# Performance work log

Measured on AMD Instinct MI355X. Metric: run time of the kernel, lower is better.

## Reference

```python
import jax, jax.numpy as jnp
import numpy as np

B, C, H, W = 2, 256, 96, 192
GROUPS = 4
K = 9  # search_window_1d = (1, 9) -> 9 candidates, x-offsets -4..4, y-offset 0


def bilinear_sample(img, coords):
    """F.grid_sample(mode='bilinear', padding_mode='zeros', align_corners=True)
    with absolute pixel coordinates (torchvision optical-flow grid_sample wrapper:
    normalize by 2*x/(W-1)-1 then grid_sample align_corners=True == identity mapping).
    img: [B, C, H, W]; coords: [B, Hg, Wg, 2] as (x, y). Returns [B, C, Hg, Wg]."""
    Bi, Ci, Hi, Wi = img.shape
    x = coords[..., 0]
    y = coords[..., 1]
    x0 = jnp.floor(x)
    y0 = jnp.floor(y)
    wx1 = x - x0
    wy1 = y - y0
    wx0 = 1.0 - wx1
    wy0 = 1.0 - wy1
    flat = img.reshape(Bi, Ci, Hi * Wi)

    def gather(ix, iy):
        valid = (ix >= 0) & (ix <= Wi - 1) & (iy >= 0) & (iy <= Hi - 1)
        ixc = jnp.clip(ix, 0, Wi - 1).astype(jnp.int32)
        iyc = jnp.clip(iy, 0, Hi - 1).astype(jnp.int32)
        idx = (iyc * Wi + ixc).reshape(Bi, 1, -1)  # [B,1,Hg*Wg]
        g = jnp.take_along_axis(flat, idx, axis=2)  # [B,C,Hg*Wg]
        g = g.reshape(Bi, Ci, *ix.shape[1:])
        return g * valid[:, None].astype(img.dtype)

    out = (gather(x0, y0) * (wx0 * wy0)[:, None]
           + gather(x0 + 1, y0) * (wx1 * wy0)[:, None]
           + gather(x0, y0 + 1) * (wx0 * wy1)[:, None]
           + gather(x0 + 1, y0 + 1) * (wx1 * wy1)[:, None])
    return out


def setup_inputs() -> dict:
    key = jax.random.key(0)
    k1, k2, k3, k4 = jax.random.split(key, 4)
    return {
        "left_feature": jax.random.normal(k1, (B, C, H, W), dtype=jnp.float32),
        "right_feature": jax.random.normal(k2, (B, C, H, W), dtype=jnp.float32),
        "flow": jax.random.normal(k3, (B, 2, H, W), dtype=jnp.float32),
        "extra_offset": jax.random.normal(k4, (B, 2 * K, H, W), dtype=jnp.float32),
    }


def reference(left_feature, right_feature, flow, extra_offset):
    Bf, Cf, Hf, Wf = left_feature.shape
    gc = Cf // GROUPS
    dt = left_feature.dtype
    # 1d window offsets: meshgrid(arange(-4,5), arange(0,1), 'xy') -> (x, 0) pairs
    xs = jnp.arange(-4, 5, dtype=dt)
    win_offs = jnp.stack([xs, jnp.zeros_like(xs)], axis=-1)  # [K,2] (x,y)
    # extra_offset: [B, K, 2, H, W] -> [B, K, H, W, 2]
    extra = extra_offset.reshape(Bf, K, 2, Hf, Wf).transpose(0, 1, 3, 4, 2)
    offsets = win_offs[None, :, None, None, :] + extra  # [B,K,H,W,2]
    # base coords grid (x, y) + flow
    yy, xx = jnp.meshgrid(jnp.arange(Hf), jnp.arange(Wf), indexing="ij")
    base = jnp.stack([xx, yy], axis=-1).astype(dt)  # [H,W,2]
    coords = base[None] + flow.transpose(0, 2, 3, 1)  # [B,H,W,2]
    coords = coords[:, None] + offsets  # [B,K,H,W,2]
    coords = coords.reshape(Bf, K * Hf, Wf, 2)
    # All groups share identical window/dilation -> sample full right feature once.
    sampled = bilinear_sample(right_feature, coords)  # [B,C,K*H,W]
    sampled = sampled.reshape(Bf, GROUPS, gc, K, Hf, Wf)
    left = left_feature.reshape(Bf, GROUPS, gc, 1, Hf, Wf)
    corr = jnp.mean(left * sampled, axis=2)  # [B,G,K,H,W]
    return corr.reshape(Bf, GROUPS * K, Hf, Wf)
```

## Files before the change

kernel.cpp:

```cpp
#include <hip/hip_runtime.h>


namespace {
constexpr int kB = 2;
constexpr int kC = 256;
constexpr int kH = 96;
constexpr int kW = 192;
constexpr int kG = 4;
constexpr int kGC = kC / kG;
constexpr int kK = 9;
constexpr int kHW = kH * kW;
constexpr size_t kPlane = (size_t)kC * kHW;
constexpr int kTransBlocks = (kHW / 64) * (kC / 64) * kB * 2;
constexpr int kPreBlocks   = (kB * kHW) / 256;
constexpr int kCorrBlocks  = kB * kHW / 8;
}

typedef _Float16 half8_t __attribute__((ext_vector_type(8)));
typedef _Float16 half4_t __attribute__((ext_vector_type(4)));
typedef _Float16 half2_t __attribute__((ext_vector_type(2)));

struct TapMeta {
  int4   off;
  float4 wgt;
};

__device__ __forceinline__ float dot8(half8_t a, half8_t b, float acc) {
#if __has_builtin(__builtin_amdgcn_fdot2)
  #pragma unroll
  for (int i = 0; i < 4; ++i) {
    half2_t a2 = {a[2 * i], a[2 * i + 1]};
    half2_t b2 = {b[2 * i], b[2 * i + 1]};
    acc = __builtin_amdgcn_fdot2(a2, b2, acc, false);
  }
#else
  #pragma unroll
  for (int i = 0; i < 8; ++i) acc += (float)a[i] * (float)b[i];
#endif
  return acc;
}

__global__ __launch_bounds__(256) void prepass_kernel(
    const float* __restrict__ left, const float* __restrict__ right,
    const float* __restrict__ flow, const float* __restrict__ extra,
    _Float16* __restrict__ left_t, _Float16* __restrict__ right_t,
    TapMeta* __restrict__ meta)
{
  __shared__ float tile[64][65];
  int id = blockIdx.x;
  if (id >= kPreBlocks) {
    int tb = id - kPreBlocks;
    int pt = tb % (kHW / 64);
    int ct = (tb / (kHW / 64)) % 4;
    int z  = tb / ((kHW / 64) * 4);
    int b  = z >> 1;
    const float* in = (z & 1) ? right : left;
    _Float16*   dst = (z & 1) ? right_t : left_t;
    int p0 = pt * 64, c0 = ct * 64;
    const float* inb = in + (size_t)b * kPlane;
    _Float16*   outb = dst + (size_t)b * kPlane;
    int t = threadIdx.x;
    int cl = t >> 2;
    int q  = t & 3;
    #pragma unroll
    for (int i = 0; i < 4; ++i) {
      int j = q + 4 * i;
      float4 v = *(const float4*)(inb + (size_t)(c0 + cl) * kHW + p0 + 4 * j);
      tile[cl][4 * j + 0] = v.x;
      tile[cl][4 * j + 1] = v.y;
      tile[cl][4 * j + 2] = v.z;
      tile[cl][4 * j + 3] = v.w;
    }
    __syncthreads();
    int pl = t >> 2;
    #pragma unroll
    for (int i = 0; i < 4; ++i) {
      int c4 = (t & 3) + 4 * i;
      half4_t hv;
      hv[0] = (_Float16)tile[4 * c4 + 0][pl];
      hv[1] = (_Float16)tile[4 * c4 + 1][pl];
      hv[2] = (_Float16)tile[4 * c4 + 2][pl];
      hv[3] = (_Float16)tile[4 * c4 + 3][pl];
      *(half4_t*)(outb + (size_t)(p0 + pl) * kC + c0 + 4 * c4) = hv;
    }
  } else {
    int t = id * 256 + threadIdx.x;
    int b = t / kHW, pix = t % kHW;
    int w = pix % kW, h = pix / kW;

    const float* flowb = flow + (size_t)b * 2 * kHW + pix;
    float bx = (float)w + flowb[0];
    float by = (float)h + flowb[kHW];
    const float* extb = extra + (size_t)b * 2 * kK * kHW + pix;

    TapMeta* mp = meta + (size_t)t * kK;
    #pragma unroll
    for (int k = 0; k < kK; ++k) {
      float xx = bx + (float)(k - 4) + extb[(size_t)(2 * k) * kHW];
      float yy = by + extb[(size_t)(2 * k + 1) * kHW];
      float xf = floorf(xx), yf = floorf(yy);
      float fx = xx - xf, fy = yy - yf;
      int ix0 = (int)xf, iy0 = (int)yf;
      int ix1 = ix0 + 1, iy1 = iy0 + 1;
      bool vx0 = (ix0 >= 0) && (ix0 < kW);
      bool vx1 = (ix1 >= 0) && (ix1 < kW);
      bool vy0 = (iy0 >= 0) && (iy0 < kH);
      bool vy1 = (iy1 >= 0) && (iy1 < kH);
      int xc0 = min(max(ix0, 0), kW - 1);
      int xc1 = min(max(ix1, 0), kW - 1);
      int yc0 = min(max(iy0, 0), kH - 1);
      int yc1 = min(max(iy1, 0), kH - 1);
      float wx0 = 1.f - fx, wy0 = 1.f - fy;
      TapMeta m;
      m.off.x = (yc0 * kW + xc0) * kC;
      m.off.y = (yc0 * kW + xc1) * kC;
      m.off.z = (yc1 * kW + xc0) * kC;
      m.off.w = (yc1 * kW + xc1) * kC;
      m.wgt.x = wx0 * wy0 * ((vx0 && vy0) ? 1.f : 0.f);
      m.wgt.y = fx  * wy0 * ((vx1 && vy0) ? 1.f : 0.f);
      m.wgt.z = wx0 * fy  * ((vx0 && vy1) ? 1.f : 0.f);
      m.wgt.w = fx  * fy  * ((vx1 && vy1) ? 1.f : 0.f);
      mp[k] = m;
    }
  }
}

__global__ __launch_bounds__(256) void corr_fp16_kernel(
    const _Float16* __restrict__ left_t, const _Float16* __restrict__ right_t,
    const TapMeta* __restrict__ meta, float* __restrict__ out)
{
  __shared__ TapMeta smeta[8 * kK];

  int sb = (blockIdx.x & 7) * (kCorrBlocks / 8) + (blockIdx.x >> 3);
  int blockPix = sb * 8;

  {
    const int4* src = (const int4*)(meta + (size_t)blockPix * kK);
    int4* dst = (int4*)smeta;
    int t = threadIdx.x;
    if (t < 144) dst[t] = src[t];
  }

  int wv   = threadIdx.x >> 6;
  int lane = threadIdx.x & 63;
  int base = blockPix + wv * 2;
  int b    = base / kHW;
  int pl0  = base % kHW;
  int p    = lane >> 5;
  int cl   = lane & 31;
  int pix  = pl0 + p;

  half8_t l8 = *(const half8_t*)(left_t + ((size_t)b * kHW + pix) * kC + cl * 8);

  const _Float16* Rb = right_t + (size_t)b * kPlane + cl * 8;

  __syncthreads();
  const TapMeta* mp = smeta + (wv * 2 + p) * kK;

  float rr[kK];

  #pragma unroll
  for (int kb = 0; kb < kK; kb += 3) {
    int4   off[3];
    float4 wv4[3];
    #pragma unroll
    for (int j = 0; j < 3; ++j) {
      off[j] = mp[kb + j].off;
      wv4[j] = mp[kb + j].wgt;
    }
    half8_t t[3][4];
    #pragma unroll
    for (int j = 0; j < 3; ++j) {
      t[j][0] = *(const half8_t*)(Rb + off[j].x);
      t[j][1] = *(const half8_t*)(Rb + off[j].y);
      t[j][2] = *(const half8_t*)(Rb + off[j].z);
      t[j][3] = *(const half8_t*)(Rb + off[j].w);
    }
    #pragma unroll
    for (int j = 0; j < 3; ++j) {
      float d00 = dot8(t[j][0], l8, 0.f);
      float d01 = dot8(t[j][1], l8, 0.f);
      float d10 = dot8(t[j][2], l8, 0.f);
      float d11 = dot8(t[j][3], l8, 0.f);
      float r = wv4[j].x * d00 + wv4[j].y * d01 + wv4[j].z * d10 + wv4[j].w * d11;
      r += __shfl_xor(r, 1);
      r += __shfl_xor(r, 2);
      r += __shfl_xor(r, 4);
      rr[kb + j] = r;
    }
  }

  int g = cl >> 3;
  if ((cl & 7) == 0) {
    float* outp = out + ((size_t)b * kG + g) * kK * kHW + pix;
    #pragma unroll
    for (int k = 0; k < kK; ++k)
      outp[(size_t)k * kHW] = rr[k] * (1.f / kGC);
  }
}

__global__ __launch_bounds__(256) void crestereo_corr_fallback(
    const float* __restrict__ left, const float* __restrict__ right,
    const float* __restrict__ flow, const float* __restrict__ extra,
    float* __restrict__ out)
{
  int t = blockIdx.x * blockDim.x + threadIdx.x;
  int w = t % kW;
  int h = (t / kW) % kH;
  int k = (t / kHW) % kK;
  int g = (t / (kHW * kK)) % kG;
  int b = t / (kHW * kK * kG);

  int pix = h * kW + w;
  const float* flowb = flow + b * 2 * kHW + pix;
  float x = (float)(w + (k - 4)) + flowb[0];
  float y = (float)h + flowb[kHW];
  const float* extb = extra + (size_t)(b * 2 * kK + 2 * k) * kHW + pix;
  x += extb[0];
  y += extb[kHW];

  float xf = floorf(x), yf = floorf(y);
  float fx = x - xf, fy = y - yf;
  int ix0 = (int)xf, iy0 = (int)yf;
  int ix1 = ix0 + 1, iy1 = iy0 + 1;
  bool vx0 = (ix0 >= 0) && (ix0 < kW);
  bool vx1 = (ix1 >= 0) && (ix1 < kW);
  bool vy0 = (iy0 >= 0) && (iy0 < kH);
  bool vy1 = (iy1 >= 0) && (iy1 < kH);
  int xc0 = min(max(ix0, 0), kW - 1);
  int xc1 = min(max(ix1, 0), kW - 1);
  int yc0 = min(max(iy0, 0), kH - 1);
  int yc1 = min(max(iy1, 0), kH - 1);
  float wx0 = 1.f - fx, wy0 = 1.f - fy;
  float w00 = wx0 * wy0 * ((vx0 && vy0) ? 1.f : 0.f);
  float w01 = fx  * wy0 * ((vx1 && vy0) ? 1.f : 0.f);
  float w10 = wx0 * fy  * ((vx0 && vy1) ? 1.f : 0.f);
  float w11 = fx  * fy  * ((vx1 && vy1) ? 1.f : 0.f);
  int idx = yc0 * kW + xc0;
  int dx  = xc1 - xc0;
  int dyw = (yc1 - yc0) * kW;

  const float* Rb = right + (size_t)(b * kC + g * kGC) * kHW + idx;
  const float* Lb = left  + (size_t)(b * kC + g * kGC) * kHW + pix;

  float acc = 0.f;
  #pragma unroll 4
  for (int c = 0; c < kGC; ++c) {
    const float* Rc = Rb + (size_t)c * kHW;
    float l   = Lb[(size_t)c * kHW];
    acc += l * (w00 * Rc[0] + w01 * Rc[dx] + w10 * Rc[dyw] + w11 * Rc[dx + dyw]);
  }
  out[(size_t)((b * kG + g) * kK + k) * kHW + pix] = acc * (1.f / kGC);
}

extern "C" void kernel_launch(void* const* d_in, const int* in_sizes, int n_in,
                              void* d_out, int out_size, void* d_ws, size_t ws_size,
                              hipStream_t stream) {
  const float* left  = (const float*)d_in[0];
  const float* right = (const float*)d_in[1];
  const float* flow  = (const float*)d_in[2];
  const float* extra = (const float*)d_in[3];
  float* out = (float*)d_out;

  size_t t_bytes = 2 * (size_t)kB * kPlane * sizeof(_Float16);
  size_t m_bytes = (size_t)kB * kHW * kK * sizeof(TapMeta);
  if (ws_size >= t_bytes + m_bytes) {
    _Float16* left_t  = (_Float16*)d_ws;
    _Float16* right_t = left_t + (size_t)kB * kPlane;
    TapMeta*  meta    = (TapMeta*)((char*)d_ws + t_bytes);

    prepass_kernel<<<kPreBlocks + kTransBlocks, 256, 0, stream>>>(
        left, right, flow, extra, left_t, right_t, meta);
    corr_fp16_kernel<<<kCorrBlocks, 256, 0, stream>>>(left_t, right_t, meta, out);
  } else {
    int total = kB * kG * kK * kH * kW;
    crestereo_corr_fallback<<<(total + 255) / 256, 256, 0, stream>>>(
        left, right, flow, extra, out);
  }
}
```

Baseline: 143.1 us.

## Compute tap metadata inside correlation kernel and widen transpose stores

Tap offsets and bilinear weights are now computed per block in the correlation kernel's shared memory, using 72 threads that each handle one (pixel, tap) pair. This replaces the global metadata buffer the prepass used to write and the correlation kernel used to re-read. The prepass becomes a pure transpose-and-convert kernel that writes 8-wide half vectors instead of 4-wide ones. This removes about 5 MB of metadata traffic and a block type from the prepass. In exchange, the correlation kernel does scattered flow/extra reads and computation before its barrier.

```diff
diff --git a/kernel.cpp b/kernel.cpp
--- a/kernel.cpp
+++ b/kernel.cpp
@@ -12,7 +12,6 @@
 constexpr int kHW = kH * kW;
 constexpr size_t kPlane = (size_t)kC * kHW;
 constexpr int kTransBlocks = (kHW / 64) * (kC / 64) * kB * 2;
-constexpr int kPreBlocks   = (kB * kHW) / 256;
 constexpr int kCorrBlocks  = kB * kHW / 8;
 }
 
@@ -42,115 +41,103 @@
 
 __global__ __launch_bounds__(256) void prepass_kernel(
     const float* __restrict__ left, const float* __restrict__ right,
-    const float* __restrict__ flow, const float* __restrict__ extra,
-    _Float16* __restrict__ left_t, _Float16* __restrict__ right_t,
-    TapMeta* __restrict__ meta)
+    _Float16* __restrict__ left_t, _Float16* __restrict__ right_t)
 {
   __shared__ float tile[64][65];
-  int id = blockIdx.x;
-  if (id >= kPreBlocks) {
-    int tb = id - kPreBlocks;
-    int pt = tb % (kHW / 64);
-    int ct = (tb / (kHW / 64)) % 4;
-    int z  = tb / ((kHW / 64) * 4);
-    int b  = z >> 1;
-    const float* in = (z & 1) ? right : left;
-    _Float16*   dst = (z & 1) ? right_t : left_t;
-    int p0 = pt * 64, c0 = ct * 64;
-    const float* inb = in + (size_t)b * kPlane;
-    _Float16*   outb = dst + (size_t)b * kPlane;
-    int t = threadIdx.x;
-    int cl = t >> 2;
-    int q  = t & 3;
-    #pragma unroll
-    for (int i = 0; i < 4; ++i) {
-      int j = q + 4 * i;
-      float4 v = *(const float4*)(inb + (size_t)(c0 + cl) * kHW + p0 + 4 * j);
-      tile[cl][4 * j + 0] = v.x;
-      tile[cl][4 * j + 1] = v.y;
-      tile[cl][4 * j + 2] = v.z;
-      tile[cl][4 * j + 3] = v.w;
-    }
-    __syncthreads();
-    int pl = t >> 2;
-    #pragma unroll
-    for (int i = 0; i < 4; ++i) {
-      int c4 = (t & 3) + 4 * i;
-      half4_t hv;
-      hv[0] = (_Float16)tile[4 * c4 + 0][pl];
-      hv[1] = (_Float16)tile[4 * c4 + 1][pl];
-      hv[2] = (_Float16)tile[4 * c4 + 2][pl];
-      hv[3] = (_Float16)tile[4 * c4 + 3][pl];
-      *(half4_t*)(outb + (size_t)(p0 + pl) * kC + c0 + 4 * c4) = hv;
-    }
-  } else {
-    int t = id * 256 + threadIdx.x;
-    int b = t / kHW, pix = t % kHW;
-    int w = pix % kW, h = pix / kW;
-
-    const float* flowb = flow + (size_t)b * 2 * kHW + pix;
+  int tb = blockIdx.x;
+  int pt = tb % (kHW / 64);
+  int ct = (tb / (kHW / 64)) % 4;
+  int z  = tb / ((kHW / 64) * 4);
+  int b  = z >> 1;
+  const float* in = (z & 1) ? right : left;
+  _Float16*   dst = (z & 1) ? right_t : left_t;
+  int p0 = pt * 64, c0 = ct * 64;
+  const float* inb = in + (size_t)b * kPlane;
+  _Float16*   outb = dst + (size_t)b * kPlane;
+  int t = threadIdx.x;
+  int cl = t >> 2;
+  int q  = t & 3;
+  #pragma unroll
+  for (int i = 0; i < 4; ++i) {
+    int j = q + 4 * i;
+    float4 v = *(const float4*)(inb + (size_t)(c0 + cl) * kHW + p0 + 4 * j);
+    tile[cl][4 * j + 0] = v.x;
+    tile[cl][4 * j + 1] = v.y;
+    tile[cl][4 * j + 2] = v.z;
+    tile[cl][4 * j + 3] = v.w;
+  }
+  __syncthreads();
+  int pl8 = t >> 3;
+  int c8  = t & 7;
+  #pragma unroll
+  for (int i = 0; i < 2; ++i) {
+    int px = pl8 + 32 * i;
+    half8_t hv;
+    #pragma unroll
+    for (int j = 0; j < 8; ++j)
+      hv[j] = (_Float16)tile[8 * c8 + j][px];
+    *(half8_t*)(outb + (size_t)(p0 + px) * kC + c0 + 8 * c8) = hv;
+  }
+}
+
+__global__ __launch_bounds__(256) void corr_fp16_kernel(
+    const _Float16* __restrict__ left_t, const _Float16* __restrict__ right_t,
+    const float* __restrict__ flow, const float* __restrict__ extra,
+    float* __restrict__ out)
+{
+  __shared__ TapMeta smeta[8 * kK];
+
+  int sb = (blockIdx.x & 7) * (kCorrBlocks / 8) + (blockIdx.x >> 3);
+  int blockPix = sb * 8;
+  int b    = blockPix / kHW;
+  int pix0 = blockPix % kHW;
+
+  int wv   = threadIdx.x >> 6;
+  int lane = threadIdx.x & 63;
+  int p    = lane >> 5;
+  int cl   = lane & 31;
+  int pix  = pix0 + wv * 2 + p;
+
+  half8_t l8 = *(const half8_t*)(left_t + ((size_t)b * kHW + pix) * kC + cl * 8);
+
+  int t = threadIdx.x;
+  if (t < 8 * kK) {
+    int px = t / kK;
+    int k  = t - px * kK;
+    int gpix = pix0 + px;
+    int w = gpix % kW, h = gpix / kW;
+
+    const float* flowb = flow + (size_t)b * 2 * kHW + gpix;
     float bx = (float)w + flowb[0];
     float by = (float)h + flowb[kHW];
-    const float* extb = extra + (size_t)b * 2 * kK * kHW + pix;
-
-    TapMeta* mp = meta + (size_t)t * kK;
-    #pragma unroll
-    for (int k = 0; k < kK; ++k) {
-      float xx = bx + (float)(k - 4) + extb[(size_t)(2 * k) * kHW];
-      float yy = by + extb[(size_t)(2 * k + 1) * kHW];
-      float xf = floorf(xx), yf = floorf(yy);
-      float fx = xx - xf, fy = yy - yf;
-      int ix0 = (int)xf, iy0 = (int)yf;
-      int ix1 = ix0 + 1, iy1 = iy0 + 1;
-      bool vx0 = (ix0 >= 0) && (ix0 < kW);
-      bool vx1 = (ix1 >= 0) && (ix1 < kW);
-      bool vy0 = (iy0 >= 0) && (iy0 < kH);
-      bool vy1 = (iy1 >= 0) && (iy1 < kH);
-      int xc0 = min(max(ix0, 0), kW - 1);
-      int xc1 = min(max(ix1, 0), kW - 1);
-      int yc0 = min(max(iy0, 0), kH - 1);
-      int yc1 = min(max(iy1, 0), kH - 1);
-      float wx0 = 1.f - fx, wy0 = 1.f - fy;
-      TapMeta m;
-      m.off.x = (yc0 * kW + xc0) * kC;
-      m.off.y = (yc0 * kW + xc1) * kC;
-      m.off.z = (yc1 * kW + xc0) * kC;
-      m.off.w = (yc1 * kW + xc1) * kC;
-      m.wgt.x = wx0 * wy0 * ((vx0 && vy0) ? 1.f : 0.f);
-      m.wgt.y = fx  * wy0 * ((vx1 && vy0) ? 1.f : 0.f);
-      m.wgt.z = wx0 * fy  * ((vx0 && vy1) ? 1.f : 0.f);
-      m.wgt.w = fx  * fy  * ((vx1 && vy1) ? 1.f : 0.f);
-      mp[k] = m;
-    }
-  }
-}
-
-__global__ __launch_bounds__(256) void corr_fp16_kernel(
-    const _Float16* __restrict__ left_t, const _Float16* __restrict__ right_t,
-    const TapMeta* __restrict__ meta, float* __restrict__ out)
-{
-  __shared__ TapMeta smeta[8 * kK];
-
-  int sb = (blockIdx.x & 7) * (kCorrBlocks / 8) + (blockIdx.x >> 3);
-  int blockPix = sb * 8;
-
-  {
-    const int4* src = (const int4*)(meta + (size_t)blockPix * kK);
-    int4* dst = (int4*)smeta;
-    int t = threadIdx.x;
-    if (t < 144) dst[t] = src[t];
-  }
-
-  int wv   = threadIdx.x >> 6;
-  int lane = threadIdx.x & 63;
-  int base = blockPix + wv * 2;
-  int b    = base / kHW;
-  int pl0  = base % kHW;
-  int p    = lane >> 5;
-  int cl   = lane & 31;
-  int pix  = pl0 + p;
-
-  half8_t l8 = *(const half8_t*)(left_t + ((size_t)b * kHW + pix) * kC + cl * 8);
+    const float* extb = extra + (size_t)b * 2 * kK * kHW + gpix;
+
+    float xx = bx + (float)(k - 4) + extb[(size_t)(2 * k) * kHW];
+    float yy = by + extb[(size_t)(2 * k + 1) * kHW];
+    float xf = floorf(xx), yf = floorf(yy);
+    float fx = xx - xf, fy = yy - yf;
+    int ix0 = (int)xf, iy0 = (int)yf;
+    int ix1 = ix0 + 1, iy1 = iy0 + 1;
+    bool vx0 = (ix0 >= 0) && (ix0 < kW);
+    bool vx1 = (ix1 >= 0) && (ix1 < kW);
+    bool vy0 = (iy0 >= 0) && (iy0 < kH);
+    bool vy1 = (iy1 >= 0) && (iy1 < kH);
+    int xc0 = min(max(ix0, 0), kW - 1);
+    int xc1 = min(max(ix1, 0), kW - 1);
+    int yc0 = min(max(iy0, 0), kH - 1);
+    int yc1 = min(max(iy1, 0), kH - 1);
+    float wx0 = 1.f - fx, wy0 = 1.f - fy;
+    TapMeta m;
+    m.off.x = (yc0 * kW + xc0) * kC;
+    m.off.y = (yc0 * kW + xc1) * kC;
+    m.off.z = (yc1 * kW + xc0) * kC;
+    m.off.w = (yc1 * kW + xc1) * kC;
+    m.wgt.x = wx0 * wy0 * ((vx0 && vy0) ? 1.f : 0.f);
+    m.wgt.y = fx  * wy0 * ((vx1 && vy0) ? 1.f : 0.f);
+    m.wgt.z = wx0 * fy  * ((vx0 && vy1) ? 1.f : 0.f);
+    m.wgt.w = fx  * fy  * ((vx1 && vy1) ? 1.f : 0.f);
+    smeta[t] = m;
+  }
 
   const _Float16* Rb = right_t + (size_t)b * kPlane + cl * 8;
 
@@ -168,20 +155,20 @@
       off[j] = mp[kb + j].off;
       wv4[j] = mp[kb + j].wgt;
     }
-    half8_t t[3][4];
+    half8_t tp[3][4];
     #pragma unroll
     for (int j = 0; j < 3; ++j) {
-      t[j][0] = *(const half8_t*)(Rb + off[j].x);
-      t[j][1] = *(const half8_t*)(Rb + off[j].y);
-      t[j][2] = *(const half8_t*)(Rb + off[j].z);
-      t[j][3] = *(const half8_t*)(Rb + off[j].w);
+      tp[j][0] = *(const half8_t*)(Rb + off[j].x);
+      tp[j][1] = *(const half8_t*)(Rb + off[j].y);
+      tp[j][2] = *(const half8_t*)(Rb + off[j].z);
+      tp[j][3] = *(const half8_t*)(Rb + off[j].w);
     }
     #pragma unroll
     for (int j = 0; j < 3; ++j) {
-      float d00 = dot8(t[j][0], l8, 0.f);
-      float d01 = dot8(t[j][1], l8, 0.f);
-      float d10 = dot8(t[j][2], l8, 0.f);
-      float d11 = dot8(t[j][3], l8, 0.f);
+      float d00 = dot8(tp[j][0], l8, 0.f);
+      float d01 = dot8(tp[j][1], l8, 0.f);
+      float d10 = dot8(tp[j][2], l8, 0.f);
+      float d11 = dot8(tp[j][3], l8, 0.f);
       float r = wv4[j].x * d00 + wv4[j].y * d01 + wv4[j].z * d10 + wv4[j].w * d11;
       r += __shfl_xor(r, 1);
       r += __shfl_xor(r, 2);
@@ -263,15 +250,13 @@
   float* out = (float*)d_out;
 
   size_t t_bytes = 2 * (size_t)kB * kPlane * sizeof(_Float16);
-  size_t m_bytes = (size_t)kB * kHW * kK * sizeof(TapMeta);
-  if (ws_size >= t_bytes + m_bytes) {
+  if (ws_size >= t_bytes) {
     _Float16* left_t  = (_Float16*)d_ws;
     _Float16* right_t = left_t + (size_t)kB * kPlane;
-    TapMeta*  meta    = (TapMeta*)((char*)d_ws + t_bytes);
-
-    prepass_kernel<<<kPreBlocks + kTransBlocks, 256, 0, stream>>>(
-        left, right, flow, extra, left_t, right_t, meta);
-    corr_fp16_kernel<<<kCorrBlocks, 256, 0, stream>>>(left_t, right_t, meta, out);
+
+    prepass_kernel<<<kTransBlocks, 256, 0, stream>>>(left, right, left_t, right_t);
+    corr_fp16_kernel<<<kCorrBlocks, 256, 0, stream>>>(
+        left_t, right_t, flow, extra, out);
   } else {
     int total = kB * kG * kK * kH * kW;
     crestereo_corr_fallback<<<(total + 255) / 256, 256, 0, stream>>>(
```

New measurement: 138.6 us. 3.1% less time.
